# Optimization experiments

Hardware: AMD Instinct MI355X
Metric: run time of the kernel (lower is better)

## Reference

```python
import jax, jax.numpy as jnp
import numpy as np

B, S, D = 2, 2048, 4096
H, KVH, HD = 32, 8, 128
ROPE_THETA = 10000.0

def setup_inputs() -> dict:
    key = jax.random.key(0)
    ks = jax.random.split(key, 5)
    x = jax.random.normal(ks[0], (B, S, D), jnp.float32)
    wq = jax.random.normal(ks[1], (D, H * HD), jnp.float32) * 0.02
    wk = jax.random.normal(ks[2], (D, KVH * HD), jnp.float32) * 0.02
    wv = jax.random.normal(ks[3], (D, KVH * HD), jnp.float32) * 0.02
    wo = jax.random.normal(ks[4], (H * HD, D), jnp.float32) * 0.02
    pos = jnp.arange(S, dtype=jnp.float32)
    inv_freq = 1.0 / (ROPE_THETA ** (jnp.arange(0, HD, 2, dtype=jnp.float32) / HD))
    freqs = pos[:, None] * inv_freq[None, :]  # [S, HD//2]
    return {"x": x, "cos": jnp.cos(freqs), "sin": jnp.sin(freqs),
            "wq": wq, "wk": wk, "wv": wv, "wo": wo, "start_pos": 0}

def _apply_rope(t, cos, sin):
    # t: [B, S, nh, HD]; rotate consecutive pairs (llama complex rotation)
    t = t.reshape(*t.shape[:-1], HD // 2, 2)
    t1, t2 = t[..., 0], t[..., 1]
    c = cos[None, :, None, :]
    s = sin[None, :, None, :]
    out = jnp.stack([t1 * c - t2 * s, t1 * s + t2 * c], axis=-1)
    return out.reshape(*out.shape[:-2], HD)

def reference(x, cos, sin, wq, wk, wv, wo, start_pos):
    b, s, _ = x.shape
    scale = 1.0 / np.sqrt(HD)
    xq = (x @ wq).reshape(b, s, H, HD)
    xk = (x @ wk).reshape(b, s, KVH, HD)
    xv = (x @ wv).reshape(b, s, KVH, HD)
    xq = _apply_rope(xq, cos, sin)
    xk = _apply_rope(xk, cos, sin)
    # start_pos == 0 prefill: cache write then read of [:s] is identity
    n_rep = H // KVH
    keys = jnp.repeat(xk, n_rep, axis=2)    # [b, s, H, HD]
    values = jnp.repeat(xv, n_rep, axis=2)
    q = xq.transpose(0, 2, 1, 3)            # [b, H, s, HD]
    k = keys.transpose(0, 2, 1, 3)
    v = values.transpose(0, 2, 1, 3)
    scores = jnp.einsum('bhqd,bhkd->bhqk', q, k) * scale
    mask = jnp.triu(jnp.full((s, s), -jnp.inf, dtype=scores.dtype), k=1)
    scores = scores + mask[None, None]
    attn = jax.nn.softmax(scores.astype(jnp.float32), axis=-1).astype(q.dtype)
    out = jnp.einsum('bhqk,bhkd->bhqd', attn, v)
    out = out.transpose(0, 2, 1, 3).reshape(b, s, H * HD)
    return out @ wo
```

## Files before the change

### kernel.cpp

```cpp
#include <hip/hip_runtime.h>

typedef __bf16 bf16_t;
typedef __bf16 bf16x8 __attribute__((ext_vector_type(8)));
typedef __bf16 bf16x4 __attribute__((ext_vector_type(4)));
typedef float  f32x4  __attribute__((ext_vector_type(4)));
typedef float  f32x16 __attribute__((ext_vector_type(16)));

#define NB   2
#define NS   2048
#define ND   4096
#define NH   32
#define NKVH 8
#define NHD  128

#define BAR()    asm volatile("s_barrier" ::: "memory")
#define LGKM0()  asm volatile("s_waitcnt lgkmcnt(0)" ::: "memory")
#define VMCNT8() asm volatile("s_waitcnt vmcnt(8)" ::: "memory")
#define VMCNT0() asm volatile("s_waitcnt vmcnt(0)" ::: "memory")

__device__ __forceinline__ void gl_lds16(const bf16_t* g, bf16_t* l) {
  __builtin_amdgcn_global_load_lds(
      (const __attribute__((address_space(1))) void*)g,
      (__attribute__((address_space(3))) void*)l, 16, 0, 0);
}

__global__ void convert_f32_bf16(const float* __restrict__ in, bf16_t* __restrict__ out, int n4) {
  int i = blockIdx.x * 256 + threadIdx.x;
  if (i < n4) {
    f32x4 v = *(const f32x4*)&in[(size_t)i * 4];
    bf16x4 o;
    #pragma unroll
    for (int j = 0; j < 4; ++j) o[j] = (bf16_t)v[j];
    *(bf16x4*)&out[(size_t)i * 4] = o;
  }
}

__global__ void transpose_convert(const float* __restrict__ in, bf16_t* __restrict__ out, int Nin) {
  __shared__ float t[32][33];
  int tx = threadIdx.x & 31, ty = threadIdx.x >> 5;
  int n0 = blockIdx.x * 32, k0 = blockIdx.y * 32;
  #pragma unroll
  for (int i = 0; i < 4; ++i)
    t[ty + i * 8][tx] = in[(size_t)(k0 + ty + i * 8) * Nin + n0 + tx];
  __syncthreads();
  #pragma unroll
  for (int i = 0; i < 4; ++i)
    out[(size_t)(n0 + ty + i * 8) * 4096 + k0 + tx] = (bf16_t)t[tx][ty + i * 8];
}

template <int F32OUT>
__global__ __launch_bounds__(512, 2) void gemm256(const bf16_t* __restrict__ A,
                                                  const bf16_t* __restrict__ Bt,
                                                  void* __restrict__ Cv, int M, int N, int K) {
  __shared__ __align__(16) bf16_t As[2][256 * 64];
  __shared__ __align__(16) bf16_t Bs[2][256 * 64];
  const int tid = threadIdx.x, lane = tid & 63, wid = tid >> 6;
  const int l31 = lane & 31, hi = lane >> 5;
  const int wm = wid >> 2, wn = wid & 3;

  const int gx = gridDim.x;
  const int nwg = gx * gridDim.y;
  const int id = blockIdx.y * gx + blockIdx.x;
  const int wg = (id & 7) * (nwg >> 3) + (id >> 3);
  const int bx = wg % gx, by = wg / gx;
  const int row0 = bx * 256, col0 = by * 256;

  const bf16_t* Ab = A + (size_t)row0 * K;
  const bf16_t* Bb = Bt + (size_t)col0 * K;

  auto stageA = [&](int t2, int buf) {
    const int k0 = t2 * 64;
    #pragma unroll
    for (int i = 0; i < 4; ++i) {
      int phys = i * 8192 + tid * 16;
      int logi = phys ^ (((phys >> 7) & 7) << 4);
      gl_lds16(Ab + (size_t)(logi >> 7) * K + k0 + ((logi & 127) >> 1), &As[buf][phys >> 1]);
    }
  };
  auto stageB = [&](int t2, int buf) {
    const int k0 = t2 * 64;
    #pragma unroll
    for (int i = 0; i < 4; ++i) {
      int phys = i * 8192 + tid * 16;
      int logi = phys ^ (((phys >> 7) & 7) << 4);
      gl_lds16(Bb + (size_t)(logi >> 7) * K + k0 + ((logi & 127) >> 1), &Bs[buf][phys >> 1]);
    }
  };

  f32x16 acc[4][2];
  #pragma unroll
  for (int m = 0; m < 4; ++m)
    #pragma unroll
    for (int n = 0; n < 2; ++n)
      #pragma unroll
      for (int r = 0; r < 16; ++r) acc[m][n][r] = 0.f;

  const int nt = K >> 6;
  stageB(0, 0); stageA(0, 0);
  stageB(1, 1); stageA(1, 1);
  VMCNT8();
  BAR();

  const int arow = wm * 128 + l31;
  const int brow = wn * 64 + l31;
  const int rsw = (l31 & 7) << 4;

  for (int t = 0; t < nt; ++t) {
    const int cur = t & 1;
    const bool pf = (t < nt - 2);
    bf16x8 a01[2][4], a23[2][4], b0[4], b1[4];

    #pragma unroll
    for (int m = 0; m < 2; ++m)
      #pragma unroll
      for (int kk = 0; kk < 4; ++kk) {
        int lb = (arow + m * 32) * 128 + kk * 32 + hi * 16;
        a01[m][kk] = *(const bf16x8*)&As[cur][(lb ^ rsw) >> 1];
      }
    #pragma unroll
    for (int kk = 0; kk < 4; ++kk) {
      int lb = brow * 128 + kk * 32 + hi * 16;
      b0[kk] = *(const bf16x8*)&Bs[cur][(lb ^ rsw) >> 1];
    }
    BAR();
    __builtin_amdgcn_s_setprio(1);
    #pragma unroll
    for (int kk = 0; kk < 4; ++kk) {
      acc[0][0] = __builtin_amdgcn_mfma_f32_32x32x16_bf16(a01[0][kk], b0[kk], acc[0][0], 0, 0, 0);
      acc[1][0] = __builtin_amdgcn_mfma_f32_32x32x16_bf16(a01[1][kk], b0[kk], acc[1][0], 0, 0, 0);
    }
    __builtin_amdgcn_s_setprio(0);
    BAR();

    #pragma unroll
    for (int kk = 0; kk < 4; ++kk) {
      int lb = (brow + 32) * 128 + kk * 32 + hi * 16;
      b1[kk] = *(const bf16x8*)&Bs[cur][(lb ^ rsw) >> 1];
    }
    BAR();
    __builtin_amdgcn_s_setprio(1);
    #pragma unroll
    for (int kk = 0; kk < 4; ++kk) {
      acc[0][1] = __builtin_amdgcn_mfma_f32_32x32x16_bf16(a01[0][kk], b1[kk], acc[0][1], 0, 0, 0);
      acc[1][1] = __builtin_amdgcn_mfma_f32_32x32x16_bf16(a01[1][kk], b1[kk], acc[1][1], 0, 0, 0);
    }
    __builtin_amdgcn_s_setprio(0);
    LGKM0();
    BAR();

    if (pf) stageB(t + 2, cur);
    #pragma unroll
    for (int m = 0; m < 2; ++m)
      #pragma unroll
      for (int kk = 0; kk < 4; ++kk) {
        int lb = (arow + 64 + m * 32) * 128 + kk * 32 + hi * 16;
        a23[m][kk] = *(const bf16x8*)&As[cur][(lb ^ rsw) >> 1];
      }
    BAR();
    __builtin_amdgcn_s_setprio(1);
    #pragma unroll
    for (int kk = 0; kk < 4; ++kk) {
      acc[2][0] = __builtin_amdgcn_mfma_f32_32x32x16_bf16(a23[0][kk], b0[kk], acc[2][0], 0, 0, 0);
      acc[3][0] = __builtin_amdgcn_mfma_f32_32x32x16_bf16(a23[1][kk], b0[kk], acc[3][0], 0, 0, 0);
    }
    __builtin_amdgcn_s_setprio(0);
    LGKM0();
    BAR();

    if (pf) stageA(t + 2, cur);
    BAR();
    __builtin_amdgcn_s_setprio(1);
    #pragma unroll
    for (int kk = 0; kk < 4; ++kk) {
      acc[2][1] = __builtin_amdgcn_mfma_f32_32x32x16_bf16(a23[0][kk], b1[kk], acc[2][1], 0, 0, 0);
      acc[3][1] = __builtin_amdgcn_mfma_f32_32x32x16_bf16(a23[1][kk], b1[kk], acc[3][1], 0, 0, 0);
    }
    __builtin_amdgcn_s_setprio(0);
    if (pf) { VMCNT8(); } else { VMCNT0(); }
    BAR();
  }

  #pragma unroll
  for (int m = 0; m < 4; ++m)
    #pragma unroll
    for (int n = 0; n < 2; ++n)
      #pragma unroll
      for (int r = 0; r < 16; ++r) {
        int rl = (r & 3) + 8 * (r >> 2) + 4 * hi;
        size_t row = (size_t)row0 + wm * 128 + m * 32 + rl;
        size_t col = (size_t)col0 + wn * 64 + n * 32 + l31;
        if (F32OUT) ((float*)Cv)[row * N + col] = acc[m][n][r];
        else ((bf16_t*)Cv)[row * N + col] = (bf16_t)acc[m][n][r];
      }
}

__global__ void rope_qk(const bf16_t* __restrict__ qkv, const float* __restrict__ cosT,
                        const float* __restrict__ sinT, bf16_t* __restrict__ Q,
                        bf16_t* __restrict__ Kout) {
  int it = blockIdx.x * 256 + threadIdx.x;
  int chunk = it & 15;
  int hs = (it >> 4) % 40;
  int m = (it >> 4) / 40;
  int b = m >> 11, srow = m & 2047;

  bf16x8 v = *(const bf16x8*)&qkv[(size_t)m * 6144 + hs * 128 + chunk * 8];
  f32x4 c4 = *(const f32x4*)&cosT[(size_t)srow * 64 + chunk * 4];
  f32x4 s4 = *(const f32x4*)&sinT[(size_t)srow * 64 + chunk * 4];
  bf16x8 o;
  #pragma unroll
  for (int j = 0; j < 4; ++j) {
    float t1 = (float)v[2 * j], t2 = (float)v[2 * j + 1];
    o[2 * j]     = (bf16_t)(t1 * c4[j] - t2 * s4[j]);
    o[2 * j + 1] = (bf16_t)(t1 * s4[j] + t2 * c4[j]);
  }
  bf16_t* dst;
  if (hs < 32) dst = Q + (((size_t)(b * 32 + hs)) * 2048 + srow) * 128 + chunk * 8;
  else         dst = Kout + (((size_t)(b * 8 + (hs - 32))) * 2048 + srow) * 128 + chunk * 8;
  *(bf16x8*)dst = o;
}

__global__ void transpose_v(const bf16_t* __restrict__ qkv, bf16_t* __restrict__ Vt) {
  __shared__ bf16_t t[32][33];
  int tx = threadIdx.x & 31, ty = threadIdx.x >> 5;
  int s0 = blockIdx.x * 32, d0 = blockIdx.y * 32, g = blockIdx.z;
  int b = g >> 3, kv = g & 7;
  const bf16_t* src = qkv + (size_t)(b * 2048) * 6144 + 5120 + kv * 128;
  #pragma unroll
  for (int i = 0; i < 4; ++i)
    t[ty + i * 8][tx] = src[(size_t)(s0 + ty + i * 8) * 6144 + d0 + tx];
  __syncthreads();
  bf16_t* dst = Vt + (size_t)g * 128 * 2048;
  #pragma unroll
  for (int i = 0; i < 4; ++i)
    dst[(size_t)(d0 + ty + i * 8) * 2048 + s0 + tx] = t[tx][ty + i * 8];
}

__global__ __launch_bounds__(512, 2) void attn_kernel(const bf16_t* __restrict__ Q,
                                                      const bf16_t* __restrict__ Kc,
                                                      const bf16_t* __restrict__ Vt,
                                                      bf16_t* __restrict__ Oout) {
  __shared__ __align__(16) bf16_t Ks[2][64 * 128];
  __shared__ __align__(16) bf16_t Vs[2][128 * 64];

  const int tid = threadIdx.x, wid = tid >> 6, lane = tid & 63;
  const int l31 = lane & 31, hi = lane >> 5;
  const int bh = blockIdx.y;
  const int b = bh >> 5, h = bh & 31, kv = h >> 2;
  const int pr = blockIdx.x;

  const bf16_t* Qp = Q + ((size_t)bh * 2048) * 128;
  const bf16_t* Kp = Kc + ((size_t)(b * 8 + kv) * 2048) * 128;
  const bf16_t* Vp = Vt + ((size_t)(b * 8 + kv) * 128) * 2048;

  const float kscale = 0.08838834764831845f * 1.44269504088896f;
  const int qoff = (wid < 4) ? wid * 32 : 224 - (wid - 4) * 32;

  auto stage = [&](int kt, int buf) {
    const int k0 = kt * 64;
    #pragma unroll
    for (int i = 0; i < 2; ++i) {
      int phys = i * 8192 + tid * 16;
      int logi = phys ^ (((phys >> 8) & 15) << 4);
      gl_lds16(Kp + (size_t)(k0 + (phys >> 8)) * 128 + ((logi & 255) >> 1), &Ks[buf][phys >> 1]);
    }
    #pragma unroll
    for (int i = 0; i < 2; ++i) {
      int phys = i * 8192 + tid * 16;
      int logi = phys ^ (((phys >> 7) & 7) << 4);
      gl_lds16(Vp + (size_t)(phys >> 7) * 2048 + k0 + ((logi & 127) >> 1), &Vs[buf][phys >> 1]);
    }
  };

  for (int half = 0; half < 2; ++half) {
    const int qt = half ? pr : 7 - pr;
    const int q0b = qt * 256;
    const int q0w = q0b + qoff;
    const int qg = q0w + l31;
    const int nkt = (qt + 1) * 4;

    bf16x8 qf[8];
    #pragma unroll
    for (int c = 0; c < 8; ++c) {
      bf16x8 t = *(const bf16x8*)&Qp[(size_t)qg * 128 + c * 16 + hi * 8];
      #pragma unroll
      for (int j = 0; j < 8; ++j) t[j] = (bf16_t)((float)t[j] * kscale);
      qf[c] = t;
    }

    f32x16 oa[4];
    #pragma unroll
    for (int nc = 0; nc < 4; ++nc)
      #pragma unroll
      for (int r = 0; r < 16; ++r) oa[nc][r] = 0.f;
    float m_old = -1e30f, lrow = 0.f;

    stage(0, 0);
    __syncthreads();

    for (int kt = 0; kt < nkt; ++kt) {
      const int k0 = kt * 64, cur = kt & 1;
      if (kt + 1 < nkt) stage(kt + 1, cur ^ 1);

      if (k0 <= q0w + 31) {
        f32x16 s0, s1;
        #pragma unroll
        for (int r = 0; r < 16; ++r) { s0[r] = 0.f; s1[r] = 0.f; }
        __builtin_amdgcn_s_setprio(1);
        #pragma unroll
        for (int c = 0; c < 8; ++c) {
          int lb0 = l31 * 256 + c * 32 + hi * 16;
          int pb0 = lb0 ^ (((lb0 >> 8) & 15) << 4);
          bf16x8 kf0 = *(const bf16x8*)&Ks[cur][pb0 >> 1];
          s0 = __builtin_amdgcn_mfma_f32_32x32x16_bf16(kf0, qf[c], s0, 0, 0, 0);
          int lb1 = (32 + l31) * 256 + c * 32 + hi * 16;
          int pb1 = lb1 ^ (((lb1 >> 8) & 15) << 4);
          bf16x8 kf1 = *(const bf16x8*)&Ks[cur][pb1 >> 1];
          s1 = __builtin_amdgcn_mfma_f32_32x32x16_bf16(kf1, qf[c], s1, 0, 0, 0);
        }
        __builtin_amdgcn_s_setprio(0);

        if (k0 + 63 > q0w) {
          #pragma unroll
          for (int r = 0; r < 16; ++r) {
            int key0 = k0 + ((r & 3) + 8 * (r >> 2)) + 4 * hi;
            if (key0 > qg) s0[r] = -1e30f;
            if (key0 + 32 > qg) s1[r] = -1e30f;
          }
        }

        float m8[8];
        #pragma unroll
        for (int j = 0; j < 8; ++j)
          m8[j] = fmaxf(fmaxf(s0[j], s0[j + 8]), fmaxf(s1[j], s1[j + 8]));
        float ma = fmaxf(fmaxf(m8[0], m8[4]), fmaxf(m8[1], m8[5]));
        float mb = fmaxf(fmaxf(m8[2], m8[6]), fmaxf(m8[3], m8[7]));
        float mh = fmaxf(ma, mb);
        float mfull = fmaxf(mh, __shfl_xor(mh, 32));
        float mn = fmaxf(m_old, mfull);
        bool nores = (mfull <= m_old);
        float sc = exp2f(m_old - mn);
        m_old = mn;

        if (!__all((int)nores)) {
          #pragma unroll
          for (int r = 0; r < 16; ++r) {
            int qi = (r & 3) + 8 * (r >> 2) + 4 * hi;
            float scv = __int_as_float(__builtin_amdgcn_ds_bpermute(qi << 2, __float_as_int(sc)));
            oa[0][r] *= scv; oa[1][r] *= scv; oa[2][r] *= scv; oa[3][r] *= scv;
          }
        }

        #pragma unroll
        for (int r = 0; r < 16; ++r) {
          s0[r] = exp2f(s0[r] - mn);
          s1[r] = exp2f(s1[r] - mn);
        }
        float rsA = 0.f, rsB = 0.f, rsC = 0.f, rsD = 0.f;
        #pragma unroll
        for (int r = 0; r < 16; r += 4) {
          rsA += s0[r];     rsB += s0[r + 1]; rsC += s0[r + 2]; rsD += s0[r + 3];
          rsA += s1[r];     rsB += s1[r + 1]; rsC += s1[r + 2]; rsD += s1[r + 3];
        }
        float rs = (rsA + rsB) + (rsC + rsD);
        rs += __shfl_xor(rs, 32);
        lrow = lrow * sc + rs;

        #pragma unroll
        for (int ks = 0; ks < 4; ++ks) {
          const int qi0 = (ks & 1) * 8;
          union { bf16_t hh[4]; int ii[2]; } ku, su;
          #pragma unroll
          for (int j = 0; j < 4; ++j) {
            float lo, hv;
            if (ks >> 1) { lo = s1[qi0 + j]; hv = s1[qi0 + 4 + j]; }
            else         { lo = s0[qi0 + j]; hv = s0[qi0 + 4 + j]; }
            ku.hh[j] = (bf16_t)(hi ? hv : lo);
            su.hh[j] = (bf16_t)(hi ? lo : hv);
          }
          int r0 = __shfl_xor(su.ii[0], 32), r1 = __shfl_xor(su.ii[1], 32);
          union { int ii[4]; bf16x8 v; } fa;
          fa.ii[0] = hi ? r0 : ku.ii[0];
          fa.ii[1] = hi ? r1 : ku.ii[1];
          fa.ii[2] = hi ? ku.ii[0] : r0;
          fa.ii[3] = hi ? ku.ii[1] : r1;
          __builtin_amdgcn_s_setprio(1);
          #pragma unroll
          for (int nc = 0; nc < 4; ++nc) {
            int lb = (nc * 32 + l31) * 128 + ks * 32 + hi * 16;
            int pb = lb ^ (((lb >> 7) & 7) << 4);
            bf16x8 vf = *(const bf16x8*)&Vs[cur][pb >> 1];
            oa[nc] = __builtin_amdgcn_mfma_f32_32x32x16_bf16(fa.v, vf, oa[nc], 0, 0, 0);
          }
          __builtin_amdgcn_s_setprio(0);
        }
      }
      __syncthreads();
    }

    float inv = 1.0f / lrow;
    bf16_t* Op = Oout + ((size_t)(b * 2048 + q0w)) * 4096 + (size_t)h * 128;
    #pragma unroll
    for (int r = 0; r < 16; ++r) {
      int qi = (r & 3) + 8 * (r >> 2) + 4 * hi;
      float iv = __int_as_float(__builtin_amdgcn_ds_bpermute(qi << 2, __float_as_int(inv)));
      #pragma unroll
      for (int nc = 0; nc < 4; ++nc)
        Op[(size_t)qi * 4096 + nc * 32 + l31] = (bf16_t)(oa[nc][r] * iv);
    }
  }
}

extern "C" void kernel_launch(void* const* d_in, const int* in_sizes, int n_in,
                              void* d_out, int out_size, void* d_ws, size_t ws_size,
                              hipStream_t stream) {
  const float* x    = (const float*)d_in[0];
  const float* cosT = (const float*)d_in[1];
  const float* sinT = (const float*)d_in[2];
  const float* wq   = (const float*)d_in[3];
  const float* wk   = (const float*)d_in[4];
  const float* wv   = (const float*)d_in[5];
  const float* wo   = (const float*)d_in[6];
  float* out = (float*)d_out;
  char* ws = (char*)d_ws;

  bf16_t* wqkvT = (bf16_t*)(ws + 0);
  bf16_t* woT   = wqkvT;
  bf16_t* xb    = (bf16_t*)(ws + 50331648);
  bf16_t* Qb    = xb;
  bf16_t* qkv   = (bf16_t*)(ws + 83886080);
  bf16_t* attn_out = qkv;
  bf16_t* Kb    = (bf16_t*)(ws + 134217728);
  bf16_t* Vt    = (bf16_t*)(ws + 142606336);

  convert_f32_bf16<<<16384, 256, 0, stream>>>(x, xb, 4194304);
  transpose_convert<<<dim3(128, 128), 256, 0, stream>>>(wq, wqkvT, 4096);
  transpose_convert<<<dim3(32, 128), 256, 0, stream>>>(wk, wqkvT + (size_t)4096 * 4096, 1024);
  transpose_convert<<<dim3(32, 128), 256, 0, stream>>>(wv, wqkvT + (size_t)5120 * 4096, 1024);

  gemm256<0><<<dim3(16, 24), 512, 0, stream>>>(xb, wqkvT, qkv, 4096, 6144, 4096);

  transpose_convert<<<dim3(128, 128), 256, 0, stream>>>(wo, woT, 4096);
  rope_qk<<<10240, 256, 0, stream>>>(qkv, cosT, sinT, Qb, Kb);
  transpose_v<<<dim3(64, 4, 16), 256, 0, stream>>>(qkv, Vt);

  attn_kernel<<<dim3(4, 64), 512, 0, stream>>>(Qb, Kb, Vt, attn_out);

  gemm256<1><<<dim3(16, 16), 512, 0, stream>>>(attn_out, woT, out, 4096, 4096, 4096);
}
```

Measured before the change: 598.1 us.

## Switch GEMM to 16x16x32 MFMA with split-half LDS tiles and new swizzle

Rewrites the 256x256 GEMM inner loop to use 16x16x32 bf16 MFMAs instead of 32x32x16. It also splits the A/B LDS tiles into two 128-row halves with a different XOR swizzle and reorders fragment loads and prefetch stages across the four compute phases. The aim is better LDS read patterns and MFMA issue within the same tile shape. The trade-off is more MFMA instructions per tile, an extra lgkmcnt wait per phase, and a less contiguous epilogue store pattern.

```diff
diff --git a/kernel.cpp b/kernel.cpp
--- a/kernel.cpp
+++ b/kernel.cpp
@@ -52,11 +52,13 @@
 __global__ __launch_bounds__(512, 2) void gemm256(const bf16_t* __restrict__ A,
                                                   const bf16_t* __restrict__ Bt,
                                                   void* __restrict__ Cv, int M, int N, int K) {
-  __shared__ __align__(16) bf16_t As[2][256 * 64];
-  __shared__ __align__(16) bf16_t Bs[2][256 * 64];
+  __shared__ __align__(16) bf16_t As[2][2][128 * 64];
+  __shared__ __align__(16) bf16_t Bs[2][2][128 * 64];
   const int tid = threadIdx.x, lane = tid & 63, wid = tid >> 6;
-  const int l31 = lane & 31, hi = lane >> 5;
+  const int l15 = lane & 15, l4 = lane >> 4;
   const int wm = wid >> 2, wn = wid & 3;
+  const int bhalf = wn >> 1;
+  const int brbase = (wn & 1) * 64;
 
   const int gx = gridDim.x;
   const int nwg = gx * gridDim.y;
@@ -68,130 +70,142 @@
   const bf16_t* Ab = A + (size_t)row0 * K;
   const bf16_t* Bb = Bt + (size_t)col0 * K;
 
-  auto stageA = [&](int t2, int buf) {
-    const int k0 = t2 * 64;
-    #pragma unroll
-    for (int i = 0; i < 4; ++i) {
+  auto stA = [&](int t, int h, int buf) {
+    #pragma unroll
+    for (int i = 0; i < 2; ++i) {
       int phys = i * 8192 + tid * 16;
-      int logi = phys ^ (((phys >> 7) & 7) << 4);
-      gl_lds16(Ab + (size_t)(logi >> 7) * K + k0 + ((logi & 127) >> 1), &As[buf][phys >> 1]);
+      int logi = phys ^ (((phys >> 8) & 7) << 4);
+      gl_lds16(Ab + (size_t)(h * 128 + (logi >> 7)) * K + t * 64 + ((logi & 127) >> 1),
+               &As[buf][h][phys >> 1]);
     }
   };
-  auto stageB = [&](int t2, int buf) {
-    const int k0 = t2 * 64;
-    #pragma unroll
-    for (int i = 0; i < 4; ++i) {
+  auto stB = [&](int t, int h, int buf) {
+    #pragma unroll
+    for (int i = 0; i < 2; ++i) {
       int phys = i * 8192 + tid * 16;
-      int logi = phys ^ (((phys >> 7) & 7) << 4);
-      gl_lds16(Bb + (size_t)(logi >> 7) * K + k0 + ((logi & 127) >> 1), &Bs[buf][phys >> 1]);
+      int logi = phys ^ (((phys >> 8) & 7) << 4);
+      gl_lds16(Bb + (size_t)(h * 128 + (logi >> 7)) * K + t * 64 + ((logi & 127) >> 1),
+               &Bs[buf][h][phys >> 1]);
     }
   };
 
-  f32x16 acc[4][2];
-  #pragma unroll
-  for (int m = 0; m < 4; ++m)
-    #pragma unroll
-    for (int n = 0; n < 2; ++n)
-      #pragma unroll
-      for (int r = 0; r < 16; ++r) acc[m][n][r] = 0.f;
+  f32x4 acc[8][4];
+  #pragma unroll
+  for (int m = 0; m < 8; ++m)
+    #pragma unroll
+    for (int n = 0; n < 4; ++n)
+      #pragma unroll
+      for (int j = 0; j < 4; ++j) acc[m][n][j] = 0.f;
 
   const int nt = K >> 6;
-  stageB(0, 0); stageA(0, 0);
-  stageB(1, 1); stageA(1, 1);
+  stA(0, 0, 0); stA(0, 1, 0); stB(0, 0, 0); stB(0, 1, 0);
+  stA(1, 0, 1); stA(1, 1, 1); stB(1, 0, 1); stB(1, 1, 1);
   VMCNT8();
   BAR();
 
-  const int arow = wm * 128 + l31;
-  const int brow = wn * 64 + l31;
-  const int rsw = (l31 & 7) << 4;
-
   for (int t = 0; t < nt; ++t) {
     const int cur = t & 1;
-    const bool pf = (t < nt - 2);
-    bf16x8 a01[2][4], a23[2][4], b0[4], b1[4];
-
-    #pragma unroll
-    for (int m = 0; m < 2; ++m)
-      #pragma unroll
-      for (int kk = 0; kk < 4; ++kk) {
-        int lb = (arow + m * 32) * 128 + kk * 32 + hi * 16;
-        a01[m][kk] = *(const bf16x8*)&As[cur][(lb ^ rsw) >> 1];
+    const bool pf = (t + 2 < nt);
+    bf16x8 a0f[4][2], a1f[4][2], b0f[2][2], b1f[2][2];
+
+    #pragma unroll
+    for (int mf = 0; mf < 4; ++mf)
+      #pragma unroll
+      for (int kh = 0; kh < 2; ++kh) {
+        int lb = (mf * 16 + l15) * 128 + kh * 64 + l4 * 16;
+        a0f[mf][kh] = *(const bf16x8*)&As[cur][wm][(lb ^ (((lb >> 8) & 7) << 4)) >> 1];
       }
     #pragma unroll
-    for (int kk = 0; kk < 4; ++kk) {
-      int lb = brow * 128 + kk * 32 + hi * 16;
-      b0[kk] = *(const bf16x8*)&Bs[cur][(lb ^ rsw) >> 1];
-    }
-    BAR();
+    for (int nf = 0; nf < 2; ++nf)
+      #pragma unroll
+      for (int kh = 0; kh < 2; ++kh) {
+        int lb = (brbase + nf * 16 + l15) * 128 + kh * 64 + l4 * 16;
+        b0f[nf][kh] = *(const bf16x8*)&Bs[cur][bhalf][(lb ^ (((lb >> 8) & 7) << 4)) >> 1];
+      }
+    BAR();
+    LGKM0();
     __builtin_amdgcn_s_setprio(1);
     #pragma unroll
-    for (int kk = 0; kk < 4; ++kk) {
-      acc[0][0] = __builtin_amdgcn_mfma_f32_32x32x16_bf16(a01[0][kk], b0[kk], acc[0][0], 0, 0, 0);
-      acc[1][0] = __builtin_amdgcn_mfma_f32_32x32x16_bf16(a01[1][kk], b0[kk], acc[1][0], 0, 0, 0);
-    }
+    for (int mf = 0; mf < 4; ++mf)
+      #pragma unroll
+      for (int nf = 0; nf < 2; ++nf)
+        #pragma unroll
+        for (int kh = 0; kh < 2; ++kh)
+          acc[mf][nf] = __builtin_amdgcn_mfma_f32_16x16x32_bf16(a0f[mf][kh], b0f[nf][kh], acc[mf][nf], 0, 0, 0);
     __builtin_amdgcn_s_setprio(0);
     BAR();
 
     #pragma unroll
-    for (int kk = 0; kk < 4; ++kk) {
-      int lb = (brow + 32) * 128 + kk * 32 + hi * 16;
-      b1[kk] = *(const bf16x8*)&Bs[cur][(lb ^ rsw) >> 1];
-    }
-    BAR();
+    for (int mf = 0; mf < 4; ++mf)
+      #pragma unroll
+      for (int kh = 0; kh < 2; ++kh) {
+        int lb = (64 + mf * 16 + l15) * 128 + kh * 64 + l4 * 16;
+        a1f[mf][kh] = *(const bf16x8*)&As[cur][wm][(lb ^ (((lb >> 8) & 7) << 4)) >> 1];
+      }
+    BAR();
+    LGKM0();
     __builtin_amdgcn_s_setprio(1);
     #pragma unroll
-    for (int kk = 0; kk < 4; ++kk) {
-      acc[0][1] = __builtin_amdgcn_mfma_f32_32x32x16_bf16(a01[0][kk], b1[kk], acc[0][1], 0, 0, 0);
-      acc[1][1] = __builtin_amdgcn_mfma_f32_32x32x16_bf16(a01[1][kk], b1[kk], acc[1][1], 0, 0, 0);
-    }
+    for (int mf = 0; mf < 4; ++mf)
+      #pragma unroll
+      for (int nf = 0; nf < 2; ++nf)
+        #pragma unroll
+        for (int kh = 0; kh < 2; ++kh)
+          acc[4 + mf][nf] = __builtin_amdgcn_mfma_f32_16x16x32_bf16(a1f[mf][kh], b0f[nf][kh], acc[4 + mf][nf], 0, 0, 0);
     __builtin_amdgcn_s_setprio(0);
+    BAR();
+
+    #pragma unroll
+    for (int nf = 0; nf < 2; ++nf)
+      #pragma unroll
+      for (int kh = 0; kh < 2; ++kh) {
+        int lb = (brbase + 32 + nf * 16 + l15) * 128 + kh * 64 + l4 * 16;
+        b1f[nf][kh] = *(const bf16x8*)&Bs[cur][bhalf][(lb ^ (((lb >> 8) & 7) << 4)) >> 1];
+      }
+    if (pf) { stA(t + 2, 0, cur); stA(t + 2, 1, cur); }
+    BAR();
     LGKM0();
-    BAR();
-
-    if (pf) stageB(t + 2, cur);
-    #pragma unroll
-    for (int m = 0; m < 2; ++m)
-      #pragma unroll
-      for (int kk = 0; kk < 4; ++kk) {
-        int lb = (arow + 64 + m * 32) * 128 + kk * 32 + hi * 16;
-        a23[m][kk] = *(const bf16x8*)&As[cur][(lb ^ rsw) >> 1];
-      }
-    BAR();
     __builtin_amdgcn_s_setprio(1);
     #pragma unroll
-    for (int kk = 0; kk < 4; ++kk) {
-      acc[2][0] = __builtin_amdgcn_mfma_f32_32x32x16_bf16(a23[0][kk], b0[kk], acc[2][0], 0, 0, 0);
-      acc[3][0] = __builtin_amdgcn_mfma_f32_32x32x16_bf16(a23[1][kk], b0[kk], acc[3][0], 0, 0, 0);
-    }
+    for (int mf = 0; mf < 4; ++mf)
+      #pragma unroll
+      for (int nf = 0; nf < 2; ++nf)
+        #pragma unroll
+        for (int kh = 0; kh < 2; ++kh)
+          acc[4 + mf][2 + nf] = __builtin_amdgcn_mfma_f32_16x16x32_bf16(a1f[mf][kh], b1f[nf][kh], acc[4 + mf][2 + nf], 0, 0, 0);
     __builtin_amdgcn_s_setprio(0);
-    LGKM0();
-    BAR();
-
-    if (pf) stageA(t + 2, cur);
-    BAR();
+    BAR();
+
+    if (pf) { stB(t + 2, 0, cur); stB(t + 2, 1, cur); }
     __builtin_amdgcn_s_setprio(1);
     #pragma unroll
-    for (int kk = 0; kk < 4; ++kk) {
-      acc[2][1] = __builtin_amdgcn_mfma_f32_32x32x16_bf16(a23[0][kk], b1[kk], acc[2][1], 0, 0, 0);
-      acc[3][1] = __builtin_amdgcn_mfma_f32_32x32x16_bf16(a23[1][kk], b1[kk], acc[3][1], 0, 0, 0);
-    }
+    for (int mf = 0; mf < 4; ++mf)
+      #pragma unroll
+      for (int nf = 0; nf < 2; ++nf)
+        #pragma unroll
+        for (int kh = 0; kh < 2; ++kh)
+          acc[mf][2 + nf] = __builtin_amdgcn_mfma_f32_16x16x32_bf16(a0f[mf][kh], b1f[nf][kh], acc[mf][2 + nf], 0, 0, 0);
     __builtin_amdgcn_s_setprio(0);
     if (pf) { VMCNT8(); } else { VMCNT0(); }
     BAR();
   }
 
   #pragma unroll
-  for (int m = 0; m < 4; ++m)
-    #pragma unroll
-    for (int n = 0; n < 2; ++n)
-      #pragma unroll
-      for (int r = 0; r < 16; ++r) {
-        int rl = (r & 3) + 8 * (r >> 2) + 4 * hi;
-        size_t row = (size_t)row0 + wm * 128 + m * 32 + rl;
-        size_t col = (size_t)col0 + wn * 64 + n * 32 + l31;
-        if (F32OUT) ((float*)Cv)[row * N + col] = acc[m][n][r];
-        else ((bf16_t*)Cv)[row * N + col] = (bf16_t)acc[m][n][r];
-      }
+  for (int mh = 0; mh < 2; ++mh)
+    #pragma unroll
+    for (int mf = 0; mf < 4; ++mf)
+      #pragma unroll
+      for (int ns = 0; ns < 2; ++ns)
+        #pragma unroll
+        for (int nf = 0; nf < 2; ++nf)
+          #pragma unroll
+          for (int r = 0; r < 4; ++r) {
+            size_t row = (size_t)row0 + wm * 128 + mh * 64 + mf * 16 + l4 * 4 + r;
+            size_t col = (size_t)col0 + wn * 64 + ns * 32 + nf * 16 + l15;
+            float v = acc[mh * 4 + mf][ns * 2 + nf][r];
+            if (F32OUT) ((float*)Cv)[row * N + col] = v;
+            else ((bf16_t*)Cv)[row * N + col] = (bf16_t)v;
+          }
 }
 
 __global__ void rope_qk(const bf16_t* __restrict__ qkv, const float* __restrict__ cosT,
```

After: 620.7 us. 3.8% more time.
